# Performance work log

Hardware: AMD Instinct MI355X
Metric: run time of the kernel (lower is better)

## Reference

```python
import jax, jax.numpy as jnp
import numpy as np

N_EXPERTS = 8
D_IN = 512
D_OUT = 512


def setup_inputs() -> dict:
    key = jax.random.key(0)
    k1, k2, k3, k4 = jax.random.split(key, 4)
    B, N = 16, 4096
    z = jax.random.randint(k1, (B, N), 0, N_EXPERTS, dtype=jnp.int64 if jax.config.jax_enable_x64 else jnp.int32)
    x = jax.random.normal(k2, (B, N, D_IN), dtype=jnp.float32)
    # Expert parameters: map_list[e] modeled as Linear(D_IN, D_OUT)
    W = jax.random.normal(k3, (N_EXPERTS, D_IN, D_OUT), dtype=jnp.float32) * (1.0 / np.sqrt(D_IN))
    b = jax.random.normal(k4, (N_EXPERTS, D_OUT), dtype=jnp.float32) * 0.01
    return {"z": z, "x": x, "W": W, "b": b}


def reference(z, x, W, b):
    B, N = z.shape
    z_flat = z.reshape(-1)                 # [T]
    x_flat = x.reshape(-1, x.shape[-1])    # [T, D_in]
    T = z_flat.shape[0]
    y = jnp.zeros((T, D_OUT), dtype=x.dtype)
    # Dense equivalent of mask-gather -> expert apply -> masked scatter.
    # Tokens with id == -1 (or any id not hit) stay zero, matching the torch code.
    for e in range(N_EXPERTS):
        mask = (z_flat == e)[:, None]      # [T, 1]
        y_e = x_flat @ W[e] + b[e]         # [T, D_out]
        y = jnp.where(mask, y_e, y)
    y = y.reshape(B, N, D_OUT)
    return (z, y)
```

## Files before the change

### kernel.cpp

```cpp
#include <hip/hip_runtime.h>
#include <stdint.h>

#define NEXP 8
#define DD   512
#define BM   128
#define BN   128
#define BK   32

typedef short s16x8 __attribute__((ext_vector_type(8)));
typedef float f32x4 __attribute__((ext_vector_type(4)));

static __device__ __forceinline__ unsigned short f2bf(float f) {
    union { float f; unsigned u; } v; v.f = f;
    unsigned r = v.u + 0x7FFFu + ((v.u >> 16) & 1u);
    return (unsigned short)(r >> 16);
}


__global__ void hist_kernel(const int* __restrict__ z, int* __restrict__ counts, int T) {
    __shared__ int lc[NEXP];
    int tid = threadIdx.x;
    if (tid < NEXP) lc[tid] = 0;
    __syncthreads();
    int t = blockIdx.x * blockDim.x + tid;
    if (t < T) atomicAdd(&lc[z[t]], 1);
    __syncthreads();
    if (tid < NEXP) atomicAdd(&counts[tid], lc[tid]);
}

__global__ void scan_kernel(const int* __restrict__ counts, int* __restrict__ cursors,
                            int4* __restrict__ table, int max_tiles) {
    if (blockIdx.x == 0 && threadIdx.x == 0) {
        int off = 0, tidx = 0;
        for (int e = 0; e < NEXP; e++) {
            cursors[e] = off;
            int c = counts[e];
            for (int r = 0; r < c; r += BM) {
                int4 ent; ent.x = e; ent.y = off + r; ent.z = c - r; ent.w = 0;
                table[tidx++] = ent;
            }
            off += c;
        }
        for (int i = tidx; i < max_tiles; i++) {
            int4 ent; ent.x = -1; ent.y = 0; ent.z = 0; ent.w = 0;
            table[i] = ent;
        }
    }
}

__global__ void scatter_kernel(const int* __restrict__ z, int* __restrict__ cursors,
                               int* __restrict__ token_index, float* __restrict__ zout, int T) {
    __shared__ int lc[NEXP];
    __shared__ int lbase[NEXP];
    int tid = threadIdx.x;
    if (tid < NEXP) lc[tid] = 0;
    __syncthreads();
    int t = blockIdx.x * blockDim.x + tid;
    int e = 0, rank = 0;
    if (t < T) {
        e = z[t];
        rank = atomicAdd(&lc[e], 1);
        zout[t] = (float)e;
    }
    __syncthreads();
    if (tid < NEXP) lbase[tid] = atomicAdd(&cursors[tid], lc[tid]);
    __syncthreads();
    if (t < T) token_index[lbase[e] + rank] = t;
}

__global__ void convw_kernel(const float* __restrict__ W, unsigned short* __restrict__ Wt) {
    __shared__ float tile[32][33];
    int e = blockIdx.z, k0 = blockIdx.x * 32, n0 = blockIdx.y * 32;
    int tid = threadIdx.x;
    const float* We = W + (size_t)e * DD * DD;
    unsigned short* WtE = Wt + (size_t)e * DD * DD;
    int c = tid & 31, r0 = tid >> 5;
#pragma unroll
    for (int i = 0; i < 4; i++) {
        int kr = r0 + 8 * i;
        tile[kr][c] = We[(size_t)(k0 + kr) * DD + n0 + c];
    }
    __syncthreads();
#pragma unroll
    for (int i = 0; i < 4; i++) {
        int nr = r0 + 8 * i;
        WtE[(size_t)(n0 + nr) * DD + k0 + c] = f2bf(tile[c][nr]);
    }
}


__global__ __launch_bounds__(256) void gemm_kernel(
    const float* __restrict__ x,
    const unsigned short* __restrict__ Wt,
    const float* __restrict__ bias,
    const int* __restrict__ token_index,
    const int4* __restrict__ table,
    float* __restrict__ y)
{
    int4 te = table[blockIdx.x];
    int e = te.x;
    if (e < 0) return;
    int base = te.y;
    int rows_valid = te.z < BM ? te.z : BM;
    int n0 = blockIdx.y * BN;

    __shared__ unsigned short Als[BM * 40];
    __shared__ unsigned short Bls[BN * 40];

    const int tid  = threadIdx.x;
    const int lane = tid & 63;
    const int wave = tid >> 6;
    const int wm = (wave & 1) * 64;
    const int wn = (wave >> 1) * 64;

    const int a_q  = tid & 7;
    const int a_r0 = tid >> 3;
    int tok[4];
#pragma unroll
    for (int i = 0; i < 4; i++) {
        int r = a_r0 + 32 * i;
        int rr = (r < rows_valid) ? r : 0;
        tok[i] = token_index[base + rr];
    }
    const int b_c  = tid & 3;
    const int b_n0 = tid >> 2;
    const unsigned short* WtE = Wt + (size_t)e * DD * DD;

    f32x4 acc[4][4];
#pragma unroll
    for (int i = 0; i < 4; i++)
#pragma unroll
        for (int j = 0; j < 4; j++) acc[i][j] = (f32x4){0.f, 0.f, 0.f, 0.f};

    const int quad = lane >> 4;
    const int lrow = lane & 15;

    for (int k0 = 0; k0 < DD; k0 += BK) {
        __syncthreads();
#pragma unroll
        for (int i = 0; i < 4; i++) {
            int r = a_r0 + 32 * i;
            const float4 v = *(const float4*)(x + (size_t)tok[i] * DD + k0 + a_q * 4);
            unsigned u0 = (unsigned)f2bf(v.x) | ((unsigned)f2bf(v.y) << 16);
            unsigned u1 = (unsigned)f2bf(v.z) | ((unsigned)f2bf(v.w) << 16);
            uint2 p; p.x = u0; p.y = u1;
            *(uint2*)(&Als[r * 40 + a_q * 4]) = p;
        }
#pragma unroll
        for (int i = 0; i < 2; i++) {
            int n = b_n0 + 64 * i;
            uint4 v = *(const uint4*)(WtE + (size_t)(n0 + n) * DD + k0 + b_c * 8);
            *(uint4*)(&Bls[n * 40 + b_c * 8]) = v;
        }
        __syncthreads();

        s16x8 af[4], bq[4];
#pragma unroll
        for (int i = 0; i < 4; i++)
            af[i] = *(const s16x8*)(&Als[(wm + i * 16 + lrow) * 40 + quad * 8]);
#pragma unroll
        for (int j = 0; j < 4; j++)
            bq[j] = *(const s16x8*)(&Bls[(wn + j * 16 + lrow) * 40 + quad * 8]);
#pragma unroll
        for (int i = 0; i < 4; i++)
#pragma unroll
            for (int j = 0; j < 4; j++)
                acc[i][j] = __builtin_amdgcn_mfma_f32_16x16x32_bf16(af[i], bq[j], acc[i][j], 0, 0, 0);
    }

    const int lcol = lane & 15;
    float bv[4];
#pragma unroll
    for (int j = 0; j < 4; j++) bv[j] = bias[e * DD + n0 + wn + j * 16 + lcol];
#pragma unroll
    for (int i = 0; i < 4; i++) {
#pragma unroll
        for (int reg = 0; reg < 4; reg++) {
            int r = wm + i * 16 + quad * 4 + reg;
            if (r < rows_valid) {
                int t = token_index[base + r];
                float* yr = y + (size_t)t * DD + n0 + wn + lcol;
#pragma unroll
                for (int j = 0; j < 4; j++)
                    yr[j * 16] = acc[i][j][reg] + bv[j];
            }
        }
    }
}


extern "C" void kernel_launch(void* const* d_in, const int* in_sizes, int n_in,
                              void* d_out, int out_size, void* d_ws, size_t ws_size,
                              hipStream_t stream) {
    const int*   z = (const int*)d_in[0];
    const float* x = (const float*)d_in[1];
    const float* W = (const float*)d_in[2];
    const float* b = (const float*)d_in[3];
    const int T = in_sizes[0];

    float* zout = (float*)d_out;
    float* y    = (float*)d_out + T;

    char* ws = (char*)d_ws;
    int*  counts      = (int*)ws;
    int*  cursors     = (int*)(ws + 32);
    int4* table       = (int4*)(ws + 256);
    int*  token_index = (int*)(ws + 16640);
    unsigned short* Wt = (unsigned short*)(ws + 294912);

    const int max_tiles = T / BM + NEXP;

    hipMemsetAsync(ws, 0, 64, stream);
    hist_kernel<<<(T + 255) / 256, 256, 0, stream>>>(z, counts, T);
    convw_kernel<<<dim3(DD / 32, DD / 32, NEXP), 256, 0, stream>>>(W, Wt);
    scan_kernel<<<1, 1, 0, stream>>>(counts, cursors, table, max_tiles);
    scatter_kernel<<<(T + 255) / 256, 256, 0, stream>>>(z, cursors, token_index, zout, T);
    gemm_kernel<<<dim3(max_tiles, DD / BN), 256, 0, stream>>>(x, Wt, b, token_index, table, y);
}
```

Baseline: 340.8 us.

## Pre-gather tokens to bf16 and use direct global-to-LDS loads in GEMM

Adds a gather kernel that converts the routed tokens to bf16 in a contiguous, expert-sorted buffer. A new GEMM kernel then streams both operands with global_load_lds into XOR-swizzled shared memory, using BK=64 with two MFMA k-steps per tile. The scan kernel becomes parallel over tile-table entries. This removes the per-block fp32 gathers and conversions from the GEMM, which were repeated across the four N-tiles, and cuts barrier count. The cost is an extra pass that writes and reads a bf16 activation buffer, and the fast path runs only if the workspace is large enough. Rows past the end of a partial tile read neighbouring or out-of-range gathered rows; those results are masked on store, but the last tile may read past the filled part of the buffer.

```diff
diff --git a/kernel.cpp b/kernel.cpp
--- a/kernel.cpp
+++ b/kernel.cpp
@@ -5,7 +5,6 @@
 #define DD   512
 #define BM   128
 #define BN   128
-#define BK   32
 
 typedef short s16x8 __attribute__((ext_vector_type(8)));
 typedef float f32x4 __attribute__((ext_vector_type(4)));
@@ -30,21 +29,31 @@
 
 __global__ void scan_kernel(const int* __restrict__ counts, int* __restrict__ cursors,
                             int4* __restrict__ table, int max_tiles) {
-    if (blockIdx.x == 0 && threadIdx.x == 0) {
-        int off = 0, tidx = 0;
+    __shared__ int off[NEXP + 1];
+    __shared__ int tb[NEXP + 1];
+    int tid = threadIdx.x;
+    if (tid == 0) {
+        int o = 0, tbs = 0;
         for (int e = 0; e < NEXP; e++) {
-            cursors[e] = off;
+            off[e] = o; tb[e] = tbs;
+            cursors[e] = o;
             int c = counts[e];
-            for (int r = 0; r < c; r += BM) {
-                int4 ent; ent.x = e; ent.y = off + r; ent.z = c - r; ent.w = 0;
-                table[tidx++] = ent;
-            }
-            off += c;
-        }
-        for (int i = tidx; i < max_tiles; i++) {
-            int4 ent; ent.x = -1; ent.y = 0; ent.z = 0; ent.w = 0;
-            table[i] = ent;
-        }
+            o += c;
+            tbs += (c + BM - 1) / BM;
+        }
+        off[NEXP] = o; tb[NEXP] = tbs;
+    }
+    __syncthreads();
+    for (int idx = tid; idx < max_tiles; idx += blockDim.x) {
+        int4 ent; ent.x = -1; ent.y = 0; ent.z = 0; ent.w = 0;
+#pragma unroll
+        for (int e = 0; e < NEXP; e++) {
+            if (idx >= tb[e] && idx < tb[e + 1]) {
+                int r = (idx - tb[e]) * BM;
+                ent.x = e; ent.y = off[e] + r; ent.z = (off[e + 1] - off[e]) - r;
+            }
+        }
+        table[idx] = ent;
     }
 }
 
@@ -66,6 +75,23 @@
     if (tid < NEXP) lbase[tid] = atomicAdd(&cursors[tid], lc[tid]);
     __syncthreads();
     if (t < T) token_index[lbase[e] + rank] = t;
+}
+
+__global__ __launch_bounds__(256) void gather_kernel(const float* __restrict__ x,
+                                                     const int* __restrict__ token_index,
+                                                     unsigned short* __restrict__ xg, int T) {
+    int i = blockIdx.x * 4 + (threadIdx.x >> 6);
+    if (i >= T) return;
+    int lane = threadIdx.x & 63;
+    int t = token_index[i];
+    const float4* src = (const float4*)(x + (size_t)t * DD) + lane * 2;
+    float4 v0 = src[0], v1 = src[1];
+    uint4 p;
+    p.x = (unsigned)f2bf(v0.x) | ((unsigned)f2bf(v0.y) << 16);
+    p.y = (unsigned)f2bf(v0.z) | ((unsigned)f2bf(v0.w) << 16);
+    p.z = (unsigned)f2bf(v1.x) | ((unsigned)f2bf(v1.y) << 16);
+    p.w = (unsigned)f2bf(v1.z) | ((unsigned)f2bf(v1.w) << 16);
+    *(uint4*)(xg + (size_t)i * DD + lane * 8) = p;
 }
 
 __global__ void convw_kernel(const float* __restrict__ W, unsigned short* __restrict__ Wt) {
@@ -89,8 +115,8 @@
 }
 
 
-__global__ __launch_bounds__(256) void gemm_kernel(
-    const float* __restrict__ x,
+__global__ __launch_bounds__(256) void gemm2_kernel(
+    const unsigned short* __restrict__ xg,
     const unsigned short* __restrict__ Wt,
     const float* __restrict__ bias,
     const int* __restrict__ token_index,
@@ -100,12 +126,12 @@
     int4 te = table[blockIdx.x];
     int e = te.x;
     if (e < 0) return;
-    int base = te.y;
-    int rows_valid = te.z < BM ? te.z : BM;
-    int n0 = blockIdx.y * BN;
-
-    __shared__ unsigned short Als[BM * 40];
-    __shared__ unsigned short Bls[BN * 40];
+    const int base = te.y;
+    const int rows_valid = te.z < BM ? te.z : BM;
+    const int n0 = blockIdx.y * BN;
+
+    __shared__ unsigned short Als[BM * 64];
+    __shared__ unsigned short Bls[BN * 64];
 
     const int tid  = threadIdx.x;
     const int lane = tid & 63;
@@ -113,6 +139,104 @@
     const int wm = (wave & 1) * 64;
     const int wn = (wave >> 1) * 64;
 
+    int srow[4], schunk[4];
+#pragma unroll
+    for (int q = 0; q < 4; q++) {
+        int s = wave * 256 + q * 64 + lane;
+        srow[q]   = s >> 3;
+        schunk[q] = (s & 7) ^ ((s >> 3) & 7);
+    }
+
+    const unsigned short* WtE = Wt + (size_t)e * DD * DD;
+
+    f32x4 acc[4][4];
+#pragma unroll
+    for (int i = 0; i < 4; i++)
+#pragma unroll
+        for (int j = 0; j < 4; j++) acc[i][j] = (f32x4){0.f, 0.f, 0.f, 0.f};
+
+    const int quad = lane >> 4;
+    const int lrow = lane & 15;
+
+    for (int k0 = 0; k0 < DD; k0 += 64) {
+        __syncthreads();
+#pragma unroll
+        for (int q = 0; q < 4; q++) {
+            const int r = srow[q], c = schunk[q];
+            const unsigned short* ga = xg + (size_t)(base + r) * DD + k0 + c * 8;
+            const unsigned short* gb = WtE + (size_t)(n0 + r) * DD + k0 + c * 8;
+            unsigned short* la = &Als[(size_t)(wave * 256 + q * 64) * 8];
+            unsigned short* lb = &Bls[(size_t)(wave * 256 + q * 64) * 8];
+            __builtin_amdgcn_global_load_lds((const __attribute__((address_space(1))) void*)ga,
+                                             (__attribute__((address_space(3))) void*)la, 16, 0, 0);
+            __builtin_amdgcn_global_load_lds((const __attribute__((address_space(1))) void*)gb,
+                                             (__attribute__((address_space(3))) void*)lb, 16, 0, 0);
+        }
+        __syncthreads();
+
+#pragma unroll
+        for (int ks = 0; ks < 2; ks++) {
+            s16x8 af[4], bq[4];
+#pragma unroll
+            for (int i = 0; i < 4; i++) {
+                int r = wm + i * 16 + lrow;
+                af[i] = *(const s16x8*)(&Als[r * 64 + (((quad + 4 * ks) ^ (r & 7)) * 8)]);
+            }
+#pragma unroll
+            for (int j = 0; j < 4; j++) {
+                int r = wn + j * 16 + lrow;
+                bq[j] = *(const s16x8*)(&Bls[r * 64 + (((quad + 4 * ks) ^ (r & 7)) * 8)]);
+            }
+#pragma unroll
+            for (int i = 0; i < 4; i++)
+#pragma unroll
+                for (int j = 0; j < 4; j++)
+                    acc[i][j] = __builtin_amdgcn_mfma_f32_16x16x32_bf16(af[i], bq[j], acc[i][j], 0, 0, 0);
+        }
+    }
+
+    const int lcol = lane & 15;
+    float bv[4];
+#pragma unroll
+    for (int j = 0; j < 4; j++) bv[j] = bias[e * DD + n0 + wn + j * 16 + lcol];
+#pragma unroll
+    for (int i = 0; i < 4; i++) {
+#pragma unroll
+        for (int reg = 0; reg < 4; reg++) {
+            int r = wm + i * 16 + quad * 4 + reg;
+            if (r < rows_valid) {
+                int t = token_index[base + r];
+                float* yr = y + (size_t)t * DD + n0 + wn + lcol;
+#pragma unroll
+                for (int j = 0; j < 4; j++)
+                    yr[j * 16] = acc[i][j][reg] + bv[j];
+            }
+        }
+    }
+}
+
+
+__global__ __launch_bounds__(256) void gemm_kernel(
+    const float* __restrict__ x, const unsigned short* __restrict__ Wt,
+    const float* __restrict__ bias, const int* __restrict__ token_index,
+    const int4* __restrict__ table, float* __restrict__ y)
+{
+    int4 te = table[blockIdx.x];
+    int e = te.x;
+    if (e < 0) return;
+    int base = te.y;
+    int rows_valid = te.z < BM ? te.z : BM;
+    int n0 = blockIdx.y * BN;
+
+    __shared__ unsigned short Als[BM * 40];
+    __shared__ unsigned short Bls[BN * 40];
+
+    const int tid  = threadIdx.x;
+    const int lane = tid & 63;
+    const int wave = tid >> 6;
+    const int wm = (wave & 1) * 64;
+    const int wn = (wave >> 1) * 64;
+
     const int a_q  = tid & 7;
     const int a_r0 = tid >> 3;
     int tok[4];
@@ -135,7 +259,7 @@
     const int quad = lane >> 4;
     const int lrow = lane & 15;
 
-    for (int k0 = 0; k0 < DD; k0 += BK) {
+    for (int k0 = 0; k0 < DD; k0 += 32) {
         __syncthreads();
 #pragma unroll
         for (int i = 0; i < 4; i++) {
@@ -203,17 +327,25 @@
 
     char* ws = (char*)d_ws;
     int*  counts      = (int*)ws;
-    int*  cursors     = (int*)(ws + 32);
+    int*  cursors     = (int*)(ws + 64);
     int4* table       = (int4*)(ws + 256);
     int*  token_index = (int*)(ws + 16640);
-    unsigned short* Wt = (unsigned short*)(ws + 294912);
+    unsigned short* Wt = (unsigned short*)(ws + 278784);
+    unsigned short* xg = (unsigned short*)(ws + 4473344);
 
     const int max_tiles = T / BM + NEXP;
+    const size_t need = 4473344 + (size_t)T * DD * 2 + 131072;
 
     hipMemsetAsync(ws, 0, 64, stream);
     hist_kernel<<<(T + 255) / 256, 256, 0, stream>>>(z, counts, T);
     convw_kernel<<<dim3(DD / 32, DD / 32, NEXP), 256, 0, stream>>>(W, Wt);
-    scan_kernel<<<1, 1, 0, stream>>>(counts, cursors, table, max_tiles);
+    scan_kernel<<<1, 256, 0, stream>>>(counts, cursors, table, max_tiles);
     scatter_kernel<<<(T + 255) / 256, 256, 0, stream>>>(z, cursors, token_index, zout, T);
-    gemm_kernel<<<dim3(max_tiles, DD / BN), 256, 0, stream>>>(x, Wt, b, token_index, table, y);
-}
+
+    if (ws_size >= need) {
+        gather_kernel<<<(T + 3) / 4, 256, 0, stream>>>(x, token_index, xg, T);
+        gemm2_kernel<<<dim3(max_tiles, DD / BN), 256, 0, stream>>>(xg, Wt, b, token_index, table, y);
+    } else {
+        gemm_kernel<<<dim3(max_tiles, DD / BN), 256, 0, stream>>>(x, Wt, b, token_index, table, y);
+    }
+}
```

New measurement: 333.7 us. 2.1% less time.
